# Kernel optimization log

Measured on AMD Instinct MI355X. Metric: run time of the kernel, lower is better.

The kernel has to match this reference:

```python
import jax, jax.numpy as jnp
import numpy as np

BN_EPS = 1e-5


def setup_inputs() -> dict:
    key = jax.random.key(0)
    k1, k2, k3, k4, k5 = jax.random.split(key, 5)
    N, C_IN = 400000, 32      # input voxels, input channels
    M, K = 100000, 32         # downsampled voxels, neighbors per voxel
    C_OUT = 64
    voxel_features = jax.random.normal(k1, (N, C_IN), dtype=jnp.float32)
    key_indices = jax.random.randint(k2, (M, K), 0, N, dtype=jnp.int32)
    # key_mask == 1 marks invalid neighbors (original: gather_indices < 0)
    key_mask = jax.random.randint(k3, (M, K), 0, 2, dtype=jnp.int32)
    W = jax.random.normal(k4, (C_OUT, C_IN), dtype=jnp.float32) * (1.0 / np.sqrt(C_IN))
    b = jax.random.normal(k5, (C_OUT,), dtype=jnp.float32) * 0.01
    bn_gamma = jnp.ones((C_OUT,), dtype=jnp.float32)
    bn_beta = jnp.zeros((C_OUT,), dtype=jnp.float32)
    bn_mean = jnp.zeros((C_OUT,), dtype=jnp.float32)
    bn_var = jnp.ones((C_OUT,), dtype=jnp.float32)
    return {"voxel_features": voxel_features, "key_indices": key_indices,
            "key_mask": key_mask, "W": W, "b": b, "bn_gamma": bn_gamma,
            "bn_beta": bn_beta, "bn_mean": bn_mean, "bn_var": bn_var}


def reference(voxel_features, key_indices, key_mask, W, b, bn_gamma, bn_beta, bn_mean, bn_var):
    # grouping_operation: gather neighbor voxel features; invalid (mask==1) -> zeros
    valid = (key_mask == 0)                              # [M, K]
    idx = jnp.maximum(key_indices, 0)                    # clamp negative indices
    gathered = voxel_features[idx]                       # [M, K, C_in]
    gathered = jnp.where(valid[..., None], gathered, 0.0)
    # Conv1d(C_in, C_out, 1): pointwise linear over channels
    proj = jnp.einsum('mkc,oc->mko', gathered, W) + b    # [M, K, C_out]
    # BatchNorm1d (inference: running stats), per output channel
    x = (proj - bn_mean) * (bn_gamma / jnp.sqrt(bn_var + BN_EPS)) + bn_beta
    x = jax.nn.relu(x)
    # down_type == 'max': max over neighbor axis (invalid columns included, as in original)
    new_features = jnp.max(x, axis=1)                    # [M, C_out]
    return new_features
```

## Files before the change

### kernel.cpp

```cpp
#include <hip/hip_runtime.h>
#include <hip/hip_bf16.h>

typedef __bf16 bf16x8 __attribute__((ext_vector_type(8)));
typedef float f32x4 __attribute__((ext_vector_type(4)));
typedef unsigned int u32;
typedef u32 u32x4 __attribute__((ext_vector_type(4)));

#define BN_EPS 1e-5f
#define RB 4

__global__ __launch_bounds__(256) void convert_kernel(
    const float* __restrict__ vf, __bf16* __restrict__ tb, int n8, int N)
{
    if (blockIdx.x == 0 && threadIdx.x < 4) {
        bf16x8 z = {};
        ((bf16x8*)(tb + (size_t)N * 32))[threadIdx.x] = z;
    }
    int i = blockIdx.x * blockDim.x + threadIdx.x;
    const int stride = gridDim.x * blockDim.x;
    for (; i < n8; i += stride) {
        const f32x4 a = ((const f32x4*)vf)[2 * i];
        const f32x4 b = ((const f32x4*)vf)[2 * i + 1];
        bf16x8 o;
        o[0]=(__bf16)a.x; o[1]=(__bf16)a.y; o[2]=(__bf16)a.z; o[3]=(__bf16)a.w;
        o[4]=(__bf16)b.x; o[5]=(__bf16)b.y; o[6]=(__bf16)b.z; o[7]=(__bf16)b.w;
        ((bf16x8*)tb)[i] = o;
    }
}

__global__ __launch_bounds__(256, 4) void down_bf16(
    const __bf16* __restrict__ tb,
    const int*   __restrict__ kidx,
    const int*   __restrict__ kmask,
    const float* __restrict__ W,
    const float* __restrict__ bias,
    const float* __restrict__ gamma,
    const float* __restrict__ beta,
    const float* __restrict__ mean,
    const float* __restrict__ var,
    float* __restrict__ out,
    int M, int N)
{
    const int lane = threadIdx.x & 63;
    const int col  = lane & 15;
    const int grp  = lane >> 4;
    const int c0   = grp << 3;

    const int waves_per_block = blockDim.x >> 6;
    const int wave_id = blockIdx.x * waves_per_block + (threadIdx.x >> 6);
    const int m0 = wave_id * RB;
    if (m0 >= M) return;

    int id[RB][2], mk[RB][2];
#pragma unroll
    for (int r = 0; r < RB; ++r) {
        int m = m0 + r; m = m < M ? m : M - 1;
        const int* ip = kidx  + (size_t)m * 32;
        const int* mp = kmask + (size_t)m * 32;
        id[r][0] = __builtin_nontemporal_load(ip + col);
        id[r][1] = __builtin_nontemporal_load(ip + col + 16);
        mk[r][0] = __builtin_nontemporal_load(mp + col);
        mk[r][1] = __builtin_nontemporal_load(mp + col + 16);
    }

    bf16x8 bfrag[4];
    float S[4], T[4];
#pragma unroll
    for (int t = 0; t < 4; ++t) {
        const int o = t * 16 + col;
        const f32x4 w0 = *(const f32x4*)(W + o * 32 + c0);
        const f32x4 w1 = *(const f32x4*)(W + o * 32 + c0 + 4);
        bf16x8 f;
        f[0]=(__bf16)w0.x; f[1]=(__bf16)w0.y; f[2]=(__bf16)w0.z; f[3]=(__bf16)w0.w;
        f[4]=(__bf16)w1.x; f[5]=(__bf16)w1.y; f[6]=(__bf16)w1.z; f[7]=(__bf16)w1.w;
        bfrag[t] = f;
        const float s = gamma[o] * rsqrtf(var[o] + BN_EPS);
        S[t] = s;
        T[t] = (bias[o] - mean[o]) * s + beta[o];
    }

    u32x4 g[RB][2];
#pragma unroll
    for (int r = 0; r < RB; ++r) {
#pragma unroll
        for (int kt = 0; kt < 2; ++kt) {
            int i = id[r][kt]; i = i < 0 ? 0 : i;
            i = (mk[r][kt] == 0) ? i : N;
            g[r][kt] = *(const u32x4*)(tb + (size_t)i * 32 + c0);
        }
    }

    const f32x4 zero4 = {0.f, 0.f, 0.f, 0.f};
#pragma unroll
    for (int r = 0; r < RB; ++r) {
        const int m = m0 + r;
        const bf16x8 a0 = __builtin_bit_cast(bf16x8, g[r][0]);
        const bf16x8 a1 = __builtin_bit_cast(bf16x8, g[r][1]);
        float myout = 0.0f;
#pragma unroll
        for (int t = 0; t < 4; ++t) {
            f32x4 d0 = __builtin_amdgcn_mfma_f32_16x16x32_bf16(a0, bfrag[t], zero4, 0, 0, 0);
            f32x4 d1 = __builtin_amdgcn_mfma_f32_16x16x32_bf16(a1, bfrag[t], zero4, 0, 0, 0);
            float v = 0.0f;
#pragma unroll
            for (int q = 0; q < 4; ++q) {
                v = fmaxf(v, d0[q] * S[t] + T[t]);
                v = fmaxf(v, d1[q] * S[t] + T[t]);
            }
            v = fmaxf(v, __shfl_xor(v, 16));
            v = fmaxf(v, __shfl_xor(v, 32));
            if (grp == t) myout = v;
        }
        if (m < M) __builtin_nontemporal_store(myout, out + (size_t)m * 64 + lane);
    }
}

__global__ __launch_bounds__(256, 4) void down_fp32(
    const float* __restrict__ vf, const int* __restrict__ kidx,
    const int* __restrict__ kmask, const float* __restrict__ W,
    const float* __restrict__ bias, const float* __restrict__ gamma,
    const float* __restrict__ beta, const float* __restrict__ mean,
    const float* __restrict__ var, float* __restrict__ out, int M)
{
    const int lane = threadIdx.x & 63;
    const int col  = lane & 15;
    const int grp  = lane >> 4;
    const int c0   = grp << 3;
    const int waves_per_block = blockDim.x >> 6;
    const int wave_id     = blockIdx.x * waves_per_block + (threadIdx.x >> 6);
    const int total_waves = gridDim.x * waves_per_block;

    bf16x8 bfrag[4];
    float S[4], T[4];
#pragma unroll
    for (int t = 0; t < 4; ++t) {
        const int o = t * 16 + col;
        const f32x4 w0 = *(const f32x4*)(W + o * 32 + c0);
        const f32x4 w1 = *(const f32x4*)(W + o * 32 + c0 + 4);
        bf16x8 f;
        f[0]=(__bf16)w0.x; f[1]=(__bf16)w0.y; f[2]=(__bf16)w0.z; f[3]=(__bf16)w0.w;
        f[4]=(__bf16)w1.x; f[5]=(__bf16)w1.y; f[6]=(__bf16)w1.z; f[7]=(__bf16)w1.w;
        bfrag[t] = f;
        const float s = gamma[o] * rsqrtf(var[o] + BN_EPS);
        S[t] = s;
        T[t] = (bias[o] - mean[o]) * s + beta[o];
    }
    const f32x4 zero4 = {0.f, 0.f, 0.f, 0.f};
    for (int m = wave_id; m < M; m += total_waves) {
        const int* idxp = kidx  + (size_t)m * 32;
        const int* mskp = kmask + (size_t)m * 32;
        bf16x8 afrag[2];
#pragma unroll
        for (int kt = 0; kt < 2; ++kt) {
            const int k = kt * 16 + col;
            int id = idxp[k]; id = id < 0 ? 0 : id;
            const float sel = (mskp[k] == 0) ? 1.0f : 0.0f;
            const float* src = vf + (size_t)id * 32 + c0;
            const f32x4 g0 = *(const f32x4*)(src);
            const f32x4 g1 = *(const f32x4*)(src + 4);
            bf16x8 a;
            a[0]=(__bf16)(g0.x*sel); a[1]=(__bf16)(g0.y*sel);
            a[2]=(__bf16)(g0.z*sel); a[3]=(__bf16)(g0.w*sel);
            a[4]=(__bf16)(g1.x*sel); a[5]=(__bf16)(g1.y*sel);
            a[6]=(__bf16)(g1.z*sel); a[7]=(__bf16)(g1.w*sel);
            afrag[kt] = a;
        }
        float myout = 0.0f;
#pragma unroll
        for (int t = 0; t < 4; ++t) {
            f32x4 d0 = __builtin_amdgcn_mfma_f32_16x16x32_bf16(afrag[0], bfrag[t], zero4, 0, 0, 0);
            f32x4 d1 = __builtin_amdgcn_mfma_f32_16x16x32_bf16(afrag[1], bfrag[t], zero4, 0, 0, 0);
            float v = 0.0f;
#pragma unroll
            for (int q = 0; q < 4; ++q) {
                v = fmaxf(v, d0[q] * S[t] + T[t]);
                v = fmaxf(v, d1[q] * S[t] + T[t]);
            }
            v = fmaxf(v, __shfl_xor(v, 16));
            v = fmaxf(v, __shfl_xor(v, 32));
            if (grp == t) myout = v;
        }
        out[(size_t)m * 64 + lane] = myout;
    }
}

extern "C" void kernel_launch(void* const* d_in, const int* in_sizes, int n_in,
                              void* d_out, int out_size, void* d_ws, size_t ws_size,
                              hipStream_t stream) {
    const float* vf    = (const float*)d_in[0];
    const int*   kidx  = (const int*)  d_in[1];
    const int*   kmask = (const int*)  d_in[2];
    const float* W     = (const float*)d_in[3];
    const float* bias  = (const float*)d_in[4];
    const float* gamma = (const float*)d_in[5];
    const float* beta  = (const float*)d_in[6];
    const float* mean  = (const float*)d_in[7];
    const float* var   = (const float*)d_in[8];
    float* out = (float*)d_out;

    const int NC = in_sizes[0];
    const int N  = NC / 32;
    const int M  = in_sizes[1] / 32;
    const size_t need = ((size_t)NC + 32) * sizeof(__bf16);

    if (ws_size >= need) {
        __bf16* tb = (__bf16*)d_ws;
        convert_kernel<<<2048, 256, 0, stream>>>(vf, tb, NC / 8, N);
        const int rows_per_block = (256 / 64) * RB;
        const int blocks = (M + rows_per_block - 1) / rows_per_block;
        down_bf16<<<blocks, 256, 0, stream>>>(tb, kidx, kmask, W, bias, gamma,
                                              beta, mean, var, out, M, N);
    } else {
        down_fp32<<<2048, 256, 0, stream>>>(vf, kidx, kmask, W, bias, gamma,
                                            beta, mean, var, out, M);
    }
}
```

Before: 62.33 us.

## Prepack weights/BN params in a setup kernel and coalesce index loads

Adds a small pack kernel that converts W to bf16 MFMA fragments and folds BN/bias into scale/shift arrays once, so each wave loads them directly instead of recomputing them. Index and mask loads are now fully coalesced across the wave and redistributed with shuffles. Rows per wave double from 4 to 8. This adds an extra kernel launch and more registers per wave, which may lower occupancy.

```diff
diff --git a/kernel.cpp b/kernel.cpp
--- a/kernel.cpp
+++ b/kernel.cpp
@@ -7,15 +7,11 @@
 typedef u32 u32x4 __attribute__((ext_vector_type(4)));
 
 #define BN_EPS 1e-5f
-#define RB 4
+#define RB 8
 
 __global__ __launch_bounds__(256) void convert_kernel(
-    const float* __restrict__ vf, __bf16* __restrict__ tb, int n8, int N)
-{
-    if (blockIdx.x == 0 && threadIdx.x < 4) {
-        bf16x8 z = {};
-        ((bf16x8*)(tb + (size_t)N * 32))[threadIdx.x] = z;
-    }
+    const float* __restrict__ vf, __bf16* __restrict__ tb, int n8)
+{
     int i = blockIdx.x * blockDim.x + threadIdx.x;
     const int stride = gridDim.x * blockDim.x;
     for (; i < n8; i += stride) {
@@ -28,43 +24,17 @@
     }
 }
 
-__global__ __launch_bounds__(256, 4) void down_bf16(
-    const __bf16* __restrict__ tb,
-    const int*   __restrict__ kidx,
-    const int*   __restrict__ kmask,
-    const float* __restrict__ W,
-    const float* __restrict__ bias,
-    const float* __restrict__ gamma,
-    const float* __restrict__ beta,
-    const float* __restrict__ mean,
-    const float* __restrict__ var,
-    float* __restrict__ out,
-    int M, int N)
-{
-    const int lane = threadIdx.x & 63;
-    const int col  = lane & 15;
-    const int grp  = lane >> 4;
-    const int c0   = grp << 3;
-
-    const int waves_per_block = blockDim.x >> 6;
-    const int wave_id = blockIdx.x * waves_per_block + (threadIdx.x >> 6);
-    const int m0 = wave_id * RB;
-    if (m0 >= M) return;
-
-    int id[RB][2], mk[RB][2];
-#pragma unroll
-    for (int r = 0; r < RB; ++r) {
-        int m = m0 + r; m = m < M ? m : M - 1;
-        const int* ip = kidx  + (size_t)m * 32;
-        const int* mp = kmask + (size_t)m * 32;
-        id[r][0] = __builtin_nontemporal_load(ip + col);
-        id[r][1] = __builtin_nontemporal_load(ip + col + 16);
-        mk[r][0] = __builtin_nontemporal_load(mp + col);
-        mk[r][1] = __builtin_nontemporal_load(mp + col + 16);
-    }
-
-    bf16x8 bfrag[4];
-    float S[4], T[4];
+__global__ __launch_bounds__(64) void pack_kernel(
+    const float* __restrict__ W, const float* __restrict__ bias,
+    const float* __restrict__ gamma, const float* __restrict__ beta,
+    const float* __restrict__ mean, const float* __restrict__ var,
+    __bf16* __restrict__ tb, u32* __restrict__ packB,
+    float* __restrict__ SP, float* __restrict__ TP, int N)
+{
+    const int lane = threadIdx.x;
+    const int col = lane & 15, grp = lane >> 4, c0 = grp << 3;
+    if (lane < 16) ((u32*)(tb + (size_t)N * 32))[lane] = 0u;
+    f32x4 s4, t4;
 #pragma unroll
     for (int t = 0; t < 4; ++t) {
         const int o = t * 16 + col;
@@ -73,22 +43,74 @@
         bf16x8 f;
         f[0]=(__bf16)w0.x; f[1]=(__bf16)w0.y; f[2]=(__bf16)w0.z; f[3]=(__bf16)w0.w;
         f[4]=(__bf16)w1.x; f[5]=(__bf16)w1.y; f[6]=(__bf16)w1.z; f[7]=(__bf16)w1.w;
-        bfrag[t] = f;
+        ((bf16x8*)packB)[t * 64 + lane] = f;
         const float s = gamma[o] * rsqrtf(var[o] + BN_EPS);
-        S[t] = s;
-        T[t] = (bias[o] - mean[o]) * s + beta[o];
+        s4[t] = s;
+        t4[t] = (bias[o] - mean[o]) * s + beta[o];
+    }
+    ((f32x4*)SP)[lane] = s4;
+    ((f32x4*)TP)[lane] = t4;
+}
+
+__global__ __launch_bounds__(256, 4) void down_bf16(
+    const __bf16* __restrict__ tb,
+    const int*   __restrict__ kidx,
+    const int*   __restrict__ kmask,
+    const u32*   __restrict__ packB,
+    const float* __restrict__ SP,
+    const float* __restrict__ TP,
+    float* __restrict__ out,
+    int M, int N)
+{
+    const int lane = threadIdx.x & 63;
+    const int col  = lane & 15;
+    const int grp  = lane >> 4;
+    const int c0   = grp << 3;
+
+    const int wave_id = blockIdx.x * (blockDim.x >> 6) + (threadIdx.x >> 6);
+    const int m0 = wave_id * RB;
+    if (m0 >= M) return;
+
+    const int elim  = M * 32 - 1;
+    const int ebase = m0 * 32 + lane;
+    int ci[4], cm[4];
+#pragma unroll
+    for (int i = 0; i < 4; ++i) {
+        int e = ebase + i * 64; e = e < elim ? e : elim;
+        ci[i] = __builtin_nontemporal_load(kidx + e);
+    }
+#pragma unroll
+    for (int i = 0; i < 4; ++i) {
+        int e = ebase + i * 64; e = e < elim ? e : elim;
+        cm[i] = __builtin_nontemporal_load(kmask + e);
+    }
+
+    bf16x8 bfrag[4];
+#pragma unroll
+    for (int t = 0; t < 4; ++t)
+        bfrag[t] = ((const bf16x8*)packB)[t * 64 + lane];
+    const f32x4 Sv = ((const f32x4*)SP)[lane];
+    const f32x4 Tv = ((const f32x4*)TP)[lane];
+
+    int fid[RB][2];
+#pragma unroll
+    for (int r = 0; r < RB; ++r) {
+#pragma unroll
+        for (int kt = 0; kt < 2; ++kt) {
+            const int srcl = ((r & 1) << 5) + (kt << 4) + col;
+            int idv = __shfl(ci[r >> 1], srcl, 64);
+            int mkv = __shfl(cm[r >> 1], srcl, 64);
+            idv = idv < 0 ? 0 : idv;
+            fid[r][kt] = (mkv == 0) ? idv : N;
+        }
     }
 
     u32x4 g[RB][2];
 #pragma unroll
-    for (int r = 0; r < RB; ++r) {
-#pragma unroll
-        for (int kt = 0; kt < 2; ++kt) {
-            int i = id[r][kt]; i = i < 0 ? 0 : i;
-            i = (mk[r][kt] == 0) ? i : N;
-            g[r][kt] = *(const u32x4*)(tb + (size_t)i * 32 + c0);
-        }
-    }
+    for (int r = 0; r < RB; ++r)
+#pragma unroll
+        for (int kt = 0; kt < 2; ++kt)
+            g[r][kt] = *(const u32x4*)(tb + (size_t)fid[r][kt] * 32 + c0);
 
     const f32x4 zero4 = {0.f, 0.f, 0.f, 0.f};
 #pragma unroll
@@ -104,8 +126,8 @@
             float v = 0.0f;
 #pragma unroll
             for (int q = 0; q < 4; ++q) {
-                v = fmaxf(v, d0[q] * S[t] + T[t]);
-                v = fmaxf(v, d1[q] * S[t] + T[t]);
+                v = fmaxf(v, d0[q] * Sv[t] + Tv[t]);
+                v = fmaxf(v, d1[q] * Sv[t] + Tv[t]);
             }
             v = fmaxf(v, __shfl_xor(v, 16));
             v = fmaxf(v, __shfl_xor(v, 32));
@@ -201,15 +223,25 @@
     const int NC = in_sizes[0];
     const int N  = NC / 32;
     const int M  = in_sizes[1] / 32;
-    const size_t need = ((size_t)NC + 32) * sizeof(__bf16);
+
+    const size_t tbBytes = ((size_t)N + 1) * 32 * sizeof(__bf16);
+    const size_t packOff = tbBytes;
+    const size_t need    = packOff + 4096 + 1024 + 1024;
 
     if (ws_size >= need) {
-        __bf16* tb = (__bf16*)d_ws;
-        convert_kernel<<<2048, 256, 0, stream>>>(vf, tb, NC / 8, N);
+        __bf16* tb    = (__bf16*)d_ws;
+        u32*    packB = (u32*)  ((char*)d_ws + packOff);
+        float*  SP    = (float*)((char*)d_ws + packOff + 4096);
+        float*  TP    = (float*)((char*)d_ws + packOff + 4096 + 1024);
+
+        pack_kernel<<<1, 64, 0, stream>>>(W, bias, gamma, beta, mean, var,
+                                          tb, packB, SP, TP, N);
+        convert_kernel<<<2048, 256, 0, stream>>>(vf, tb, NC / 8);
+
         const int rows_per_block = (256 / 64) * RB;
         const int blocks = (M + rows_per_block - 1) / rows_per_block;
-        down_bf16<<<blocks, 256, 0, stream>>>(tb, kidx, kmask, W, bias, gamma,
-                                              beta, mean, var, out, M, N);
+        down_bf16<<<blocks, 256, 0, stream>>>(tb, kidx, kmask, packB, SP, TP,
+                                              out, M, N);
     } else {
         down_fp32<<<2048, 256, 0, stream>>>(vf, kidx, kmask, W, bias, gamma,
                                             beta, mean, var, out, M);
```

Result: faster. 58.23 us (-6.6%).
